# Kernel optimization log

Hardware: AMD Instinct MI355X
Metric: run time of the kernel (lower is better)

The kernel has to match this reference:

```python
import jax, jax.numpy as jnp
import numpy as np

N_PRED = 29
F_DIM = 8192
H1 = 256
H2 = 128


def setup_inputs() -> dict:
    key = jax.random.key(0)
    ks = jax.random.split(key, 7)
    features = jax.random.normal(ks[0], (4096, F_DIM), dtype=jnp.float32)
    # Stacked per-predicate MLP weights (PyTorch Linear init scale ~ 1/sqrt(fan_in))
    W1 = jax.random.normal(ks[1], (N_PRED, F_DIM, H1), dtype=jnp.float32) / np.sqrt(F_DIM)
    b1 = jax.random.normal(ks[2], (N_PRED, H1), dtype=jnp.float32) / np.sqrt(F_DIM)
    W2 = jax.random.normal(ks[3], (N_PRED, H1, H2), dtype=jnp.float32) / np.sqrt(H1)
    b2 = jax.random.normal(ks[4], (N_PRED, H2), dtype=jnp.float32) / np.sqrt(H1)
    W3 = jax.random.normal(ks[5], (N_PRED, H2), dtype=jnp.float32) / np.sqrt(H2)
    b3 = jax.random.normal(ks[6], (N_PRED,), dtype=jnp.float32) / np.sqrt(H2)
    return {"features": features, "W1": W1, "b1": b1, "W2": W2, "b2": b2, "W3": W3, "b3": b3}


def reference(features, W1, b1, W2, b2, W3, b3):
    # 29 parallel heads as one batched (grouped) GEMM chain; dropout = identity (eval).
    h1 = jax.nn.relu(jnp.einsum('bf,pfh->bph', features, W1) + b1[None])   # [B, P, H1]
    h2 = jax.nn.relu(jnp.einsum('bph,phk->bpk', h1, W2) + b2[None])        # [B, P, H2]
    logits = jnp.einsum('bpk,pk->bp', h2, W3) + b3[None]                   # [B, P]
    return jax.nn.sigmoid(logits)
```

## Files before the change

kernel.cpp:

```cpp
#include <hip/hip_runtime.h>
#include <hip/hip_bf16.h>

typedef __attribute__((ext_vector_type(8))) short short8_t;
typedef __attribute__((ext_vector_type(8))) __bf16 bf16x8;
typedef __attribute__((ext_vector_type(4))) float f32x4;

__device__ __forceinline__ void gload16(const void* g, void* l) {
  __builtin_amdgcn_global_load_lds(
      (const __attribute__((address_space(1))) void*)g,
      (__attribute__((address_space(3))) void*)l, 16, 0, 0);
}

__device__ __forceinline__ unsigned short f2bf(float f) {
  __hip_bfloat16 h = __float2bfloat16(f);
  return __builtin_bit_cast(unsigned short, h);
}

#define BARRIER() asm volatile("s_barrier" ::: "memory")


__global__ void k_cvt_feat(const float* __restrict__ in, unsigned short* __restrict__ out) {
  const size_t N = (size_t)4096 * 8192;
  size_t i = ((size_t)blockIdx.x * 256 + threadIdx.x) * 4;
  const size_t stride = (size_t)gridDim.x * 256 * 4;
  for (; i < N; i += stride) {
    float4 v = *(const float4*)(in + i);
    ushort4 o;
    o.x = f2bf(v.x); o.y = f2bf(v.y); o.z = f2bf(v.z); o.w = f2bf(v.w);
    *(ushort4*)(out + i) = o;
  }
}

__global__ void k_cvt_w1(const float* __restrict__ W1, unsigned short* __restrict__ out, int p0) {
  __shared__ unsigned short t[64][65];
  const int p = p0 + blockIdx.z;
  const float* src = W1 + (size_t)p * 8192 * 256;
  unsigned short* dst = out + (size_t)blockIdx.z * 256 * 8192;
  const int f0 = blockIdx.x * 64, h0 = blockIdx.y * 64;
#pragma unroll
  for (int i = 0; i < 16; ++i) {
    int tt = i * 256 + threadIdx.x;
    int r = tt >> 6, c = tt & 63;
    t[r][c] = f2bf(src[(size_t)(f0 + r) * 256 + h0 + c]);
  }
  __syncthreads();
#pragma unroll
  for (int i = 0; i < 4; ++i) {
    int tt = i * 256 + threadIdx.x;
    int r = tt >> 4;
    int c4 = (tt & 15) * 4;
    ushort4 o;
    o.x = t[c4][r]; o.y = t[c4 + 1][r]; o.z = t[c4 + 2][r]; o.w = t[c4 + 3][r];
    *(ushort4*)&dst[(size_t)(h0 + r) * 8192 + f0 + c4] = o;
  }
}

__global__ void k_cvt_w2(const float* __restrict__ W2, unsigned short* __restrict__ out) {
  const int p = blockIdx.x;
  const float* src = W2 + (size_t)p * 256 * 128;
  unsigned short* dst = out + (size_t)p * 128 * 256;
  for (int tt = threadIdx.x; tt < 128 * 256; tt += 256) {
    int j = tt >> 8, h = tt & 255;
    dst[tt] = f2bf(src[(size_t)h * 128 + j]);
  }
}

__global__ __launch_bounds__(512, 2) void k_gemm1(
    const unsigned short* __restrict__ A,
    const unsigned short* __restrict__ Bt,
    const float* __restrict__ b1,
    unsigned short* __restrict__ h1,
    int p0) {
  __shared__ __align__(16) unsigned short S[65536];

  const int tid = threadIdx.x;
  const int lane = tid & 63;
  const int wave = tid >> 6;
  const int sr = (wave >> 2) * 64;
  const int sc = (wave & 3) * 32;

  const int nwg = gridDim.x * gridDim.y;
  const int orig = blockIdx.y * gridDim.x + blockIdx.x;
  const int q = nwg >> 3, r_ = nwg & 7;
  const int xcd = orig & 7, idx = orig >> 3;
  const int wg = (xcd < r_ ? xcd * (q + 1) : r_ * (q + 1) + (xcd - r_) * q) + idx;
  const int mx = wg & 15;
  const int z = wg >> 4;
  const int p = p0 + z;
  const int m0 = mx * 256;

  const unsigned short* Ab = A + (size_t)m0 * 8192;
  const unsigned short* Bb = Bt + (size_t)z * 256 * 8192;

  int e0 = tid, r0 = e0 >> 3, u0 = (e0 & 7) ^ (r0 & 7);
  int e1 = 512 + tid, r1e = e1 >> 3, u1 = (e1 & 7) ^ (r1e & 7);
  const size_t s0 = (size_t)r0 * 8192 + u0 * 8;
  const size_t s1 = (size_t)r1e * 8192 + u1 * 8;
  const int ld0 = (wave * 64) * 8;
  const int ld1 = (512 + wave * 64) * 8;

  auto stage = [&](int buf, int isB, int h, int T) {
    const unsigned short* gb = (isB ? Bb : Ab) + (size_t)h * 128 * 8192 + (size_t)T * 64;
    unsigned short* lb = S + buf * 32768 + isB * 16384 + h * 8192;
    gload16(gb + s0, lb + ld0);
    gload16(gb + s1, lb + ld1);
  };

  const int l15 = lane & 15, ks = lane >> 4;

  auto rdA = [&](int buf, int h, int mi, int x) {
    int R = sr + mi * 16 + l15;
    int pu = (x * 4 + ks) ^ (R & 7);
    return __builtin_bit_cast(bf16x8, *(const short8_t*)(S + buf * 32768 + h * 8192 + R * 64 + pu * 8));
  };
  auto rdB = [&](int buf, int v, int nj, int x) {
    int R = sc + nj * 16 + l15;
    int pu = (x * 4 + ks) ^ (R & 7);
    return __builtin_bit_cast(bf16x8, *(const short8_t*)(S + buf * 32768 + 16384 + v * 8192 + R * 64 + pu * 8));
  };

  f32x4 acc[4][4][2] = {};
  const int NT = 8192 / 64;

  auto kstep = [&](int t, int pfa, int pf, int vm) {
    const int c = t & 1, nx = c ^ 1;
    bf16x8 a[4][2], bl[2][2], bh[2][2];
#pragma unroll
    for (int mi = 0; mi < 4; ++mi) { a[mi][0] = rdA(c, 0, mi, 0); a[mi][1] = rdA(c, 0, mi, 1); }
#pragma unroll
    for (int nj = 0; nj < 2; ++nj) { bl[nj][0] = rdB(c, 0, nj, 0); bl[nj][1] = rdB(c, 0, nj, 1); }
    if (pfa) stage(nx, 0, 1, t + 1);
    BARRIER();
    __builtin_amdgcn_s_setprio(1);
#pragma unroll
    for (int mi = 0; mi < 4; ++mi)
#pragma unroll
      for (int nj = 0; nj < 2; ++nj) {
        acc[0][mi][nj] = __builtin_amdgcn_mfma_f32_16x16x32_bf16(a[mi][0], bl[nj][0], acc[0][mi][nj], 0, 0, 0);
        acc[0][mi][nj] = __builtin_amdgcn_mfma_f32_16x16x32_bf16(a[mi][1], bl[nj][1], acc[0][mi][nj], 0, 0, 0);
      }
    __builtin_amdgcn_s_setprio(0);
    BARRIER();
#pragma unroll
    for (int nj = 0; nj < 2; ++nj) { bh[nj][0] = rdB(c, 1, nj, 0); bh[nj][1] = rdB(c, 1, nj, 1); }
    if (pf) stage(c, 0, 0, t + 2);
    BARRIER();
    __builtin_amdgcn_s_setprio(1);
#pragma unroll
    for (int mi = 0; mi < 4; ++mi)
#pragma unroll
      for (int nj = 0; nj < 2; ++nj) {
        acc[1][mi][nj] = __builtin_amdgcn_mfma_f32_16x16x32_bf16(a[mi][0], bh[nj][0], acc[1][mi][nj], 0, 0, 0);
        acc[1][mi][nj] = __builtin_amdgcn_mfma_f32_16x16x32_bf16(a[mi][1], bh[nj][1], acc[1][mi][nj], 0, 0, 0);
      }
    __builtin_amdgcn_s_setprio(0);
    BARRIER();
#pragma unroll
    for (int mi = 0; mi < 4; ++mi) { a[mi][0] = rdA(c, 1, mi, 0); a[mi][1] = rdA(c, 1, mi, 1); }
    if (pf) stage(c, 1, 1, t + 2);
    BARRIER();
    __builtin_amdgcn_s_setprio(1);
#pragma unroll
    for (int mi = 0; mi < 4; ++mi)
#pragma unroll
      for (int nj = 0; nj < 2; ++nj) {
        acc[2][mi][nj] = __builtin_amdgcn_mfma_f32_16x16x32_bf16(a[mi][0], bl[nj][0], acc[2][mi][nj], 0, 0, 0);
        acc[2][mi][nj] = __builtin_amdgcn_mfma_f32_16x16x32_bf16(a[mi][1], bl[nj][1], acc[2][mi][nj], 0, 0, 0);
      }
    __builtin_amdgcn_s_setprio(0);
    BARRIER();
    if (pf) stage(c, 1, 0, t + 2);
    __builtin_amdgcn_s_setprio(1);
#pragma unroll
    for (int mi = 0; mi < 4; ++mi)
#pragma unroll
      for (int nj = 0; nj < 2; ++nj) {
        acc[3][mi][nj] = __builtin_amdgcn_mfma_f32_16x16x32_bf16(a[mi][0], bh[nj][0], acc[3][mi][nj], 0, 0, 0);
        acc[3][mi][nj] = __builtin_amdgcn_mfma_f32_16x16x32_bf16(a[mi][1], bh[nj][1], acc[3][mi][nj], 0, 0, 0);
      }
    __builtin_amdgcn_s_setprio(0);
    if (vm == 6)      asm volatile("s_waitcnt vmcnt(6)" ::: "memory");
    else if (vm == 0) asm volatile("s_waitcnt vmcnt(0)" ::: "memory");
    BARRIER();
  };

  stage(0, 0, 0, 0); stage(0, 1, 0, 0); stage(0, 1, 1, 0); stage(0, 0, 1, 0);
  stage(1, 0, 0, 1); stage(1, 1, 1, 1); stage(1, 1, 0, 1);
  asm volatile("s_waitcnt vmcnt(6)" ::: "memory");
  BARRIER();

  for (int t = 0; t < NT - 2; ++t) kstep(t, 1, 1, 6);
  kstep(NT - 2, 1, 0, 0);
  kstep(NT - 1, 0, 0, -1);

  const int rg = lane >> 4;
#pragma unroll
  for (int qh = 0; qh < 2; ++qh)
#pragma unroll
    for (int qv = 0; qv < 2; ++qv) {
      const int qq = qh * 2 + qv;
#pragma unroll
      for (int nj = 0; nj < 2; ++nj) {
        const int col = qv * 128 + sc + nj * 16 + l15;
        const float bb = b1[p * 256 + col];
#pragma unroll
        for (int mi = 0; mi < 4; ++mi) {
          const int rbase = m0 + qh * 128 + sr + mi * 16 + rg * 4;
#pragma unroll
          for (int rr = 0; rr < 4; ++rr) {
            float v = acc[qq][mi][nj][rr] + bb;
            v = v > 0.f ? v : 0.f;
            h1[((size_t)p * 4096 + rbase + rr) * 256 + col] = f2bf(v);
          }
        }
      }
    }
}

__global__ __launch_bounds__(256, 2) void k_gemm23(
    const unsigned short* __restrict__ h1,
    const unsigned short* __restrict__ W2t,
    const float* __restrict__ b2,
    const float* __restrict__ W3,
    const float* __restrict__ b3,
    float* __restrict__ out) {
  __shared__ __align__(16) unsigned short lds_a[128 * 64];
  __shared__ __align__(16) unsigned short lds_b[128 * 64];
  const int tid = threadIdx.x;
  const int lane = tid & 63;
  const int wave = tid >> 6;
  const int m0 = blockIdx.x * 128;
  const int p = blockIdx.y;

  const unsigned short* Ab = h1 + ((size_t)p * 4096 + m0) * 256;
  const unsigned short* Bb = W2t + (size_t)p * 128 * 256;

  f32x4 acc[2][8] = {};

  for (int k0 = 0; k0 < 256; k0 += 64) {
    __syncthreads();
#pragma unroll
    for (int i = 0; i < 4; ++i) {
      int t = i * 256 + tid;
      int r = t >> 3;
      int uu = (t & 7) ^ (r & 7);
      gload16(Ab + (size_t)r * 256 + k0 + uu * 8, &lds_a[(i * 256 + wave * 64) * 8]);
      gload16(Bb + (size_t)r * 256 + k0 + uu * 8, &lds_b[(i * 256 + wave * 64) * 8]);
    }
    __syncthreads();
#pragma unroll
    for (int kk = 0; kk < 64; kk += 32) {
      const int ku = (kk >> 3) + (lane >> 4);
      bf16x8 af[2], bfv[8];
#pragma unroll
      for (int mi = 0; mi < 2; ++mi) {
        int row = wave * 32 + mi * 16 + (lane & 15);
        int u = ku ^ (row & 7);
        af[mi] = __builtin_bit_cast(bf16x8, *(const short8_t*)&lds_a[row * 64 + u * 8]);
      }
#pragma unroll
      for (int nj = 0; nj < 8; ++nj) {
        int row = nj * 16 + (lane & 15);
        int u = ku ^ (row & 7);
        bfv[nj] = __builtin_bit_cast(bf16x8, *(const short8_t*)&lds_b[row * 64 + u * 8]);
      }
#pragma unroll
      for (int mi = 0; mi < 2; ++mi)
#pragma unroll
        for (int nj = 0; nj < 8; ++nj)
          acc[mi][nj] = __builtin_amdgcn_mfma_f32_16x16x32_bf16(af[mi], bfv[nj], acc[mi][nj], 0, 0, 0);
    }
  }

  float b2v[8], w3v[8];
  const int c16 = lane & 15;
#pragma unroll
  for (int nj = 0; nj < 8; ++nj) {
    int c = nj * 16 + c16;
    b2v[nj] = b2[p * 128 + c];
    w3v[nj] = W3[p * 128 + c];
  }
  const float b3p = b3[p];
#pragma unroll
  for (int mi = 0; mi < 2; ++mi) {
#pragma unroll
    for (int r = 0; r < 4; ++r) {
      float s = 0.f;
#pragma unroll
      for (int nj = 0; nj < 8; ++nj) {
        float v = acc[mi][nj][r] + b2v[nj];
        v = v > 0.f ? v : 0.f;
        s += v * w3v[nj];
      }
      s += __shfl_xor(s, 1);
      s += __shfl_xor(s, 2);
      s += __shfl_xor(s, 4);
      s += __shfl_xor(s, 8);
      if ((lane & 15) == 0) {
        int m = m0 + wave * 32 + mi * 16 + (lane >> 4) * 4 + r;
        float logit = s + b3p;
        out[(size_t)m * 29 + p] = 1.f / (1.f + __expf(-logit));
      }
    }
  }
}

extern "C" void kernel_launch(void* const* d_in, const int* in_sizes, int n_in,
                              void* d_out, int out_size, void* d_ws, size_t ws_size,
                              hipStream_t stream) {
  const float* features = (const float*)d_in[0];
  const float* W1 = (const float*)d_in[1];
  const float* b1 = (const float*)d_in[2];
  const float* W2 = (const float*)d_in[3];
  const float* b2 = (const float*)d_in[4];
  const float* W3 = (const float*)d_in[5];
  const float* b3 = (const float*)d_in[6];
  float* out = (float*)d_out;

  char* ws = (char*)d_ws;
  const size_t featB = (size_t)4096 * 8192 * 2;
  const size_t h1B   = (size_t)29 * 4096 * 256 * 2;
  const size_t w2B   = (size_t)29 * 128 * 256 * 2;
  const size_t w1pp  = (size_t)256 * 8192 * 2;

  unsigned short* featbf = (unsigned short*)ws;
  unsigned short* h1bf   = (unsigned short*)(ws + featB);
  unsigned short* w2t    = (unsigned short*)(ws + featB + h1B);
  unsigned short* w1t    = (unsigned short*)(ws + featB + h1B + w2B);

  size_t base = featB + h1B + w2B;
  size_t rem = (ws_size > base) ? (ws_size - base) : 0;
  int CH = (int)(rem / w1pp);
  if (CH > 29) CH = 29;
  if (CH < 1) CH = 1;

  k_cvt_feat<<<2048, 256, 0, stream>>>(features, featbf);
  k_cvt_w2<<<29, 256, 0, stream>>>(W2, w2t);

  for (int p0 = 0; p0 < 29; p0 += CH) {
    int c = (29 - p0) < CH ? (29 - p0) : CH;
    k_cvt_w1<<<dim3(128, 4, c), 256, 0, stream>>>(W1, w1t, p0);
    k_gemm1<<<dim3(16, c), 512, 0, stream>>>(featbf, w1t, b1, h1bf, p0);
  }

  k_gemm23<<<dim3(32, 29), 256, 0, stream>>>(h1bf, w2t, b2, W3, b3, out);
}
```

Before: 540.2 us.

## Fuse second and third MLP layers into GEMM1 epilogue via LDS-staged h1

The h1 activations are no longer written to global memory. After the first GEMM, each block stages its 256x256 bf16 h1 tile in shared memory with an XOR swizzle. It then runs the 256->128 layer (W2 read straight from global with register double-buffering), the W3 dot product and the sigmoid in the same kernel, and the separate k_gemm23 launch is removed. This drops roughly 60 MB of h1 write plus read-back and one kernel launch. The W1 transpose/convert kernel is also widened to 256-feature tiles with 16-byte stores. In exchange, the GEMM1 epilogue becomes longer and register-heavy, which could affect occupancy.

```diff
diff --git a/kernel.cpp b/kernel.cpp
--- a/kernel.cpp
+++ b/kernel.cpp
@@ -32,26 +32,27 @@
 }
 
 __global__ void k_cvt_w1(const float* __restrict__ W1, unsigned short* __restrict__ out, int p0) {
-  __shared__ unsigned short t[64][65];
+  __shared__ unsigned short t[64][262];
   const int p = p0 + blockIdx.z;
   const float* src = W1 + (size_t)p * 8192 * 256;
   unsigned short* dst = out + (size_t)blockIdx.z * 256 * 8192;
-  const int f0 = blockIdx.x * 64, h0 = blockIdx.y * 64;
-#pragma unroll
-  for (int i = 0; i < 16; ++i) {
+  const int f0 = blockIdx.x * 256, h0 = blockIdx.y * 64;
+#pragma unroll
+  for (int i = 0; i < 64; ++i) {
     int tt = i * 256 + threadIdx.x;
-    int r = tt >> 6, c = tt & 63;
-    t[r][c] = f2bf(src[(size_t)(f0 + r) * 256 + h0 + c]);
+    int f = tt >> 6, c = tt & 63;
+    t[c][f] = f2bf(src[(size_t)(f0 + f) * 256 + h0 + c]);
   }
   __syncthreads();
 #pragma unroll
-  for (int i = 0; i < 4; ++i) {
+  for (int i = 0; i < 8; ++i) {
     int tt = i * 256 + threadIdx.x;
-    int r = tt >> 4;
-    int c4 = (tt & 15) * 4;
-    ushort4 o;
-    o.x = t[c4][r]; o.y = t[c4 + 1][r]; o.z = t[c4 + 2][r]; o.w = t[c4 + 3][r];
-    *(ushort4*)&dst[(size_t)(h0 + r) * 8192 + f0 + c4] = o;
+    int r = tt >> 5;
+    int c8 = (tt & 31) * 8;
+    short8_t o;
+#pragma unroll
+    for (int j = 0; j < 8; ++j) o[j] = (short)t[r][c8 + j];
+    *(short8_t*)&dst[(size_t)(h0 + r) * 8192 + f0 + c8] = o;
   }
 }
 
@@ -69,7 +70,11 @@
     const unsigned short* __restrict__ A,
     const unsigned short* __restrict__ Bt,
     const float* __restrict__ b1,
-    unsigned short* __restrict__ h1,
+    const unsigned short* __restrict__ W2t,
+    const float* __restrict__ b2,
+    const float* __restrict__ W3,
+    const float* __restrict__ b3,
+    float* __restrict__ out,
     int p0) {
   __shared__ __align__(16) unsigned short S[65536];
 
@@ -193,113 +198,91 @@
   kstep(NT - 2, 1, 0, 0);
   kstep(NT - 1, 0, 0, -1);
 
-  const int rg = lane >> 4;
-#pragma unroll
-  for (int qh = 0; qh < 2; ++qh)
-#pragma unroll
-    for (int qv = 0; qv < 2; ++qv) {
-      const int qq = qh * 2 + qv;
-#pragma unroll
-      for (int nj = 0; nj < 2; ++nj) {
-        const int col = qv * 128 + sc + nj * 16 + l15;
-        const float bb = b1[p * 256 + col];
-#pragma unroll
-        for (int mi = 0; mi < 4; ++mi) {
-          const int rbase = m0 + qh * 128 + sr + mi * 16 + rg * 4;
-#pragma unroll
-          for (int rr = 0; rr < 4; ++rr) {
-            float v = acc[qq][mi][nj][rr] + bb;
-            v = v > 0.f ? v : 0.f;
-            h1[((size_t)p * 4096 + rbase + rr) * 256 + col] = f2bf(v);
+  __syncthreads();
+  {
+    const int rg = lane >> 4;
+#pragma unroll
+    for (int qh = 0; qh < 2; ++qh)
+#pragma unroll
+      for (int qv = 0; qv < 2; ++qv) {
+        const int qq = qh * 2 + qv;
+#pragma unroll
+        for (int nj = 0; nj < 2; ++nj) {
+          const int c = qv * 128 + sc + nj * 16 + l15;
+          const float bb = b1[p * 256 + c];
+          const int u = c >> 3, sub = c & 7;
+#pragma unroll
+          for (int mi = 0; mi < 4; ++mi) {
+            const int Rb = qh * 128 + sr + mi * 16 + rg * 4;
+#pragma unroll
+            for (int rr = 0; rr < 4; ++rr) {
+              const int R = Rb + rr;
+              float v = acc[qq][mi][nj][rr] + bb;
+              v = v > 0.f ? v : 0.f;
+              S[R * 256 + ((u ^ (R & 7)) * 8) + sub] = f2bf(v);
+            }
           }
         }
       }
+  }
+  __syncthreads();
+  {
+    const unsigned short* Wp = W2t + (size_t)p * 128 * 256;
+    f32x4 acc2[2][8] = {};
+    bf16x8 bcur[8], bnxt[8];
+#pragma unroll
+    for (int nj = 0; nj < 8; ++nj)
+      bcur[nj] = __builtin_bit_cast(bf16x8, *(const short8_t*)(Wp + (nj * 16 + l15) * 256 + ks * 8));
+#pragma unroll
+    for (int kt = 0; kt < 8; ++kt) {
+      if (kt < 7) {
+#pragma unroll
+        for (int nj = 0; nj < 8; ++nj)
+          bnxt[nj] = __builtin_bit_cast(bf16x8, *(const short8_t*)(Wp + (nj * 16 + l15) * 256 + (kt + 1) * 32 + ks * 8));
+      }
+      bf16x8 a2[2];
+#pragma unroll
+      for (int mi = 0; mi < 2; ++mi) {
+        const int R = wave * 32 + mi * 16 + l15;
+        const int u = kt * 4 + ks;
+        a2[mi] = __builtin_bit_cast(bf16x8, *(const short8_t*)(S + R * 256 + ((u ^ (R & 7)) * 8)));
+      }
+#pragma unroll
+      for (int mi = 0; mi < 2; ++mi)
+#pragma unroll
+        for (int nj = 0; nj < 8; ++nj)
+          acc2[mi][nj] = __builtin_amdgcn_mfma_f32_16x16x32_bf16(a2[mi], bcur[nj], acc2[mi][nj], 0, 0, 0);
+#pragma unroll
+      for (int nj = 0; nj < 8; ++nj) bcur[nj] = bnxt[nj];
     }
-}
-
-__global__ __launch_bounds__(256, 2) void k_gemm23(
-    const unsigned short* __restrict__ h1,
-    const unsigned short* __restrict__ W2t,
-    const float* __restrict__ b2,
-    const float* __restrict__ W3,
-    const float* __restrict__ b3,
-    float* __restrict__ out) {
-  __shared__ __align__(16) unsigned short lds_a[128 * 64];
-  __shared__ __align__(16) unsigned short lds_b[128 * 64];
-  const int tid = threadIdx.x;
-  const int lane = tid & 63;
-  const int wave = tid >> 6;
-  const int m0 = blockIdx.x * 128;
-  const int p = blockIdx.y;
-
-  const unsigned short* Ab = h1 + ((size_t)p * 4096 + m0) * 256;
-  const unsigned short* Bb = W2t + (size_t)p * 128 * 256;
-
-  f32x4 acc[2][8] = {};
-
-  for (int k0 = 0; k0 < 256; k0 += 64) {
-    __syncthreads();
-#pragma unroll
-    for (int i = 0; i < 4; ++i) {
-      int t = i * 256 + tid;
-      int r = t >> 3;
-      int uu = (t & 7) ^ (r & 7);
-      gload16(Ab + (size_t)r * 256 + k0 + uu * 8, &lds_a[(i * 256 + wave * 64) * 8]);
-      gload16(Bb + (size_t)r * 256 + k0 + uu * 8, &lds_b[(i * 256 + wave * 64) * 8]);
+    float b2v[8], w3v[8];
+#pragma unroll
+    for (int nj = 0; nj < 8; ++nj) {
+      int c = nj * 16 + l15;
+      b2v[nj] = b2[p * 128 + c];
+      w3v[nj] = W3[p * 128 + c];
     }
-    __syncthreads();
-#pragma unroll
-    for (int kk = 0; kk < 64; kk += 32) {
-      const int ku = (kk >> 3) + (lane >> 4);
-      bf16x8 af[2], bfv[8];
-#pragma unroll
-      for (int mi = 0; mi < 2; ++mi) {
-        int row = wave * 32 + mi * 16 + (lane & 15);
-        int u = ku ^ (row & 7);
-        af[mi] = __builtin_bit_cast(bf16x8, *(const short8_t*)&lds_a[row * 64 + u * 8]);
-      }
-#pragma unroll
-      for (int nj = 0; nj < 8; ++nj) {
-        int row = nj * 16 + (lane & 15);
-        int u = ku ^ (row & 7);
-        bfv[nj] = __builtin_bit_cast(bf16x8, *(const short8_t*)&lds_b[row * 64 + u * 8]);
-      }
-#pragma unroll
-      for (int mi = 0; mi < 2; ++mi)
-#pragma unroll
-        for (int nj = 0; nj < 8; ++nj)
-          acc[mi][nj] = __builtin_amdgcn_mfma_f32_16x16x32_bf16(af[mi], bfv[nj], acc[mi][nj], 0, 0, 0);
-    }
-  }
-
-  float b2v[8], w3v[8];
-  const int c16 = lane & 15;
-#pragma unroll
-  for (int nj = 0; nj < 8; ++nj) {
-    int c = nj * 16 + c16;
-    b2v[nj] = b2[p * 128 + c];
-    w3v[nj] = W3[p * 128 + c];
-  }
-  const float b3p = b3[p];
-#pragma unroll
-  for (int mi = 0; mi < 2; ++mi) {
-#pragma unroll
-    for (int r = 0; r < 4; ++r) {
-      float s = 0.f;
-#pragma unroll
-      for (int nj = 0; nj < 8; ++nj) {
-        float v = acc[mi][nj][r] + b2v[nj];
-        v = v > 0.f ? v : 0.f;
-        s += v * w3v[nj];
-      }
-      s += __shfl_xor(s, 1);
-      s += __shfl_xor(s, 2);
-      s += __shfl_xor(s, 4);
-      s += __shfl_xor(s, 8);
-      if ((lane & 15) == 0) {
-        int m = m0 + wave * 32 + mi * 16 + (lane >> 4) * 4 + r;
-        float logit = s + b3p;
-        out[(size_t)m * 29 + p] = 1.f / (1.f + __expf(-logit));
+    const float b3p = b3[p];
+#pragma unroll
+    for (int mi = 0; mi < 2; ++mi) {
+#pragma unroll
+      for (int r = 0; r < 4; ++r) {
+        float s = 0.f;
+#pragma unroll
+        for (int nj = 0; nj < 8; ++nj) {
+          float v = acc2[mi][nj][r] + b2v[nj];
+          v = v > 0.f ? v : 0.f;
+          s += v * w3v[nj];
+        }
+        s += __shfl_xor(s, 1);
+        s += __shfl_xor(s, 2);
+        s += __shfl_xor(s, 4);
+        s += __shfl_xor(s, 8);
+        if (l15 == 0) {
+          int m = m0 + wave * 32 + mi * 16 + ks * 4 + r;
+          float logit = s + b3p;
+          out[(size_t)m * 29 + p] = 1.f / (1.f + __expf(-logit));
+        }
       }
     }
   }
@@ -319,16 +302,14 @@
 
   char* ws = (char*)d_ws;
   const size_t featB = (size_t)4096 * 8192 * 2;
-  const size_t h1B   = (size_t)29 * 4096 * 256 * 2;
   const size_t w2B   = (size_t)29 * 128 * 256 * 2;
   const size_t w1pp  = (size_t)256 * 8192 * 2;
 
   unsigned short* featbf = (unsigned short*)ws;
-  unsigned short* h1bf   = (unsigned short*)(ws + featB);
-  unsigned short* w2t    = (unsigned short*)(ws + featB + h1B);
-  unsigned short* w1t    = (unsigned short*)(ws + featB + h1B + w2B);
-
-  size_t base = featB + h1B + w2B;
+  unsigned short* w2t    = (unsigned short*)(ws + featB);
+  unsigned short* w1t    = (unsigned short*)(ws + featB + w2B);
+
+  size_t base = featB + w2B;
   size_t rem = (ws_size > base) ? (ws_size - base) : 0;
   int CH = (int)(rem / w1pp);
   if (CH > 29) CH = 29;
@@ -339,9 +320,7 @@
 
   for (int p0 = 0; p0 < 29; p0 += CH) {
     int c = (29 - p0) < CH ? (29 - p0) : CH;
-    k_cvt_w1<<<dim3(128, 4, c), 256, 0, stream>>>(W1, w1t, p0);
-    k_gemm1<<<dim3(16, c), 512, 0, stream>>>(featbf, w1t, b1, h1bf, p0);
-  }
-
-  k_gemm23<<<dim3(32, 29), 256, 0, stream>>>(h1bf, w2t, b2, W3, b3, out);
-}
+    k_cvt_w1<<<dim3(32, 4, c), 256, 0, stream>>>(W1, w1t, p0);
+    k_gemm1<<<dim3(16, c), 512, 0, stream>>>(featbf, w1t, b1, w2t, b2, W3, b3, out, p0);
+  }
+}
```

Result: no change. 547.0 us (+1.3%).
